# Kernel optimization log

Hardware: AMD Instinct MI355X
Metric: run time of the kernel (lower is better)

Reference implementation:

```python
import jax, jax.numpy as jnp
import numpy as np

STATE_DIM = 512
N_AGENTS = 16
N_ACTIONS = 32
EMBED = 512          # mixing_embed_dim
Q_IN = STATE_DIM + N_AGENTS * N_ACTIONS  # 1024 (coma_critic arch)
ROWS = 32768         # bs * ts = 64 * 512


def _linear_params(key, d_in, d_out):
    kw, kb = jax.random.split(key)
    bound = 1.0 / np.sqrt(d_in)
    W = jax.random.uniform(kw, (d_in, d_out), minval=-bound, maxval=bound, dtype=jnp.float32)
    b = jax.random.uniform(kb, (d_out,), minval=-bound, maxval=bound, dtype=jnp.float32)
    return W, b


def setup_inputs() -> dict:
    key = jax.random.key(0)
    ks = jax.random.split(key, 8)
    states = jax.random.normal(ks[0], (ROWS, STATE_DIM), dtype=jnp.float32)
    actions = jax.random.uniform(ks[1], (ROWS, N_AGENTS * N_ACTIONS), dtype=jnp.float32)
    Qw1, Qb1 = _linear_params(ks[2], Q_IN, EMBED)
    Qw2, Qb2 = _linear_params(ks[3], EMBED, EMBED)
    Qw3, Qb3 = _linear_params(ks[4], EMBED, 1)
    Vw1, Vb1 = _linear_params(ks[5], STATE_DIM, EMBED)
    Vw2, Vb2 = _linear_params(ks[6], EMBED, EMBED)
    Vw3, Vb3 = _linear_params(ks[7], EMBED, 1)
    return {
        "states": states, "actions": actions,
        "Qw1": Qw1, "Qb1": Qb1, "Qw2": Qw2, "Qb2": Qb2, "Qw3": Qw3, "Qb3": Qb3,
        "Vw1": Vw1, "Vb1": Vb1, "Vw2": Vw2, "Vb2": Vb2, "Vw3": Vw3, "Vb3": Vb3,
    }


def _mlp3(x, W1, b1, W2, b2, W3, b3):
    h = jax.nn.relu(x @ W1 + b1)
    h = jax.nn.relu(h @ W2 + b2)
    return h @ W3 + b3


def reference(states, actions,
              Qw1, Qb1, Qw2, Qb2, Qw3, Qb3,
              Vw1, Vb1, Vw2, Vb2, Vw3, Vb3):
    # coma_critic arch: inputs = cat([states, joint-action one-hots], dim=1)
    inputs = jnp.concatenate([states, actions], axis=1)  # [bs*ts, Q_IN]
    q_outputs = _mlp3(inputs, Qw1, Qb1, Qw2, Qb2, Qw3, Qb3)  # [bs*ts, 1]
    v_outputs = _mlp3(states, Vw1, Vb1, Vw2, Vb2, Vw3, Vb3)  # [bs*ts, 1]
    return q_outputs, v_outputs
```

## Files before the change

### kernel.cpp

```cpp
#include <hip/hip_runtime.h>


#define ROWS 32768
#define EMBED 512

using frag_ab = __attribute__((ext_vector_type(8))) short;
using f32x4   = __attribute__((ext_vector_type(4))) float;

__device__ __forceinline__ unsigned short f2bf(float f) {
    unsigned int u = __builtin_bit_cast(unsigned int, f);
    return (unsigned short)((u + 0x7fffu + ((u >> 16) & 1u)) >> 16);
}

__device__ __forceinline__ unsigned pk2(float lo, float hi) {
    return __builtin_amdgcn_perm(__builtin_bit_cast(unsigned, hi),
                                 __builtin_bit_cast(unsigned, lo), 0x07060302u);
}

__device__ __forceinline__ void async_copy16(const void* g, void* l) {
    __builtin_amdgcn_global_load_lds(
        (const __attribute__((address_space(1))) unsigned int*)g,
        (__attribute__((address_space(3))) unsigned int*)l, 16, 0, 0);
}

__global__ void init_out(float* __restrict__ out,
                         const float* __restrict__ qb3,
                         const float* __restrict__ vb3) {
    int i = blockIdx.x * 256 + threadIdx.x;
    out[i] = (i < ROWS) ? qb3[0] : vb3[0];
}

__global__ void prep_w(const float* __restrict__ Qw1, const float* __restrict__ Qw2,
                       const float* __restrict__ Vw1, const float* __restrict__ Vw2,
                       unsigned short* __restrict__ Qw1t, unsigned short* __restrict__ Qw2t,
                       unsigned short* __restrict__ Vw1t, unsigned short* __restrict__ Vw2t) {
    int t = blockIdx.x * 256 + threadIdx.x;
    if (t < 512 * 1024) {
        int n = t >> 10, k = t & 1023;
        Qw1t[t] = f2bf(Qw1[(size_t)k * 512 + n]);
    } else {
        t -= 512 * 1024;
        int seg = t >> 18;
        int r = t & 0x3ffff;
        int n = r >> 9, k = r & 511;
        const float* W = (seg == 0) ? Qw2 : (seg == 1) ? Vw1 : Vw2;
        unsigned short* O = (seg == 0) ? Qw2t : (seg == 1) ? Vw1t : Vw2t;
        O[r] = f2bf(W[(size_t)k * 512 + n]);
    }
}

__global__ __launch_bounds__(256)
void layer1(const float* __restrict__ states, const float* __restrict__ actions,
            const unsigned short* __restrict__ Qw1t,
            const unsigned short* __restrict__ Vw1t,
            const float* __restrict__ Qb1, const float* __restrict__ Vb1,
            unsigned short* __restrict__ h1Q, unsigned short* __restrict__ h1V) {
    __shared__ __align__(16) unsigned short As[128 * 40];
    __shared__ __align__(16) unsigned short Bs[128 * 32];

    const int tid = threadIdx.x, wave = tid >> 6, lane = tid & 63;
    const bool isV = blockIdx.x >= 4;
    const int bn = (blockIdx.x & 3) * 128;
    const int bm = blockIdx.y * 128;
    const int K   = isV ? 512 : 1024;
    const int ldb = isV ? 512 : 1024;
    const unsigned short* Wt = isV ? Vw1t : Qw1t;
    const float* bias = isV ? Vb1 : Qb1;
    unsigned short* H = isV ? h1V : h1Q;

    const int wm = (wave & 1) * 64, wn = (wave >> 1) * 64;
    const int lrow = lane & 15, quad = lane >> 4;
    f32x4 acc[4][4] = {};

    const int lin  = wave * 1024 + lane * 16;
    const int rowS = lin >> 6, colS = (lin & 63) >> 1;
    const unsigned short* gB0 = Wt + (size_t)(bn + rowS)      * ldb + colS;
    const unsigned short* gB1 = Wt + (size_t)(bn + rowS + 64) * ldb + colS;
    unsigned short* ldsB0 = Bs + wave * 512;
    unsigned short* ldsB1 = Bs + 2048 + wave * 512;

    const int arow = tid >> 1, ahalf = tid & 1;
    const size_t rowOff = (size_t)(bm + arow) * 512 + ahalf * 16;
    unsigned short* wp = As + arow * 40 + ahalf * 16;

    float4 f0, f1, f2, f3;
    { const float4* g = (const float4*)(states + rowOff);
      f0 = g[0]; f1 = g[1]; f2 = g[2]; f3 = g[3]; }

    for (int k0 = 0; k0 < K; k0 += 32) {
        async_copy16(gB0, ldsB0);
        async_copy16(gB1, ldsB1);
        gB0 += 32; gB1 += 32;
        uint4 w0 = make_uint4(pk2(f0.x, f0.y), pk2(f0.z, f0.w),
                              pk2(f1.x, f1.y), pk2(f1.z, f1.w));
        uint4 w1 = make_uint4(pk2(f2.x, f2.y), pk2(f2.z, f2.w),
                              pk2(f3.x, f3.y), pk2(f3.z, f3.w));
        *(uint4*)wp       = w0;
        *(uint4*)(wp + 8) = w1;
        __syncthreads();

        const int kn = k0 + 32;
        if (kn < K) {
            const float* Ab = (kn < 512) ? states : actions;
            const float4* g = (const float4*)(Ab + rowOff + (kn & 511));
            f0 = g[0]; f1 = g[1]; f2 = g[2]; f3 = g[3];
        }

        frag_ab af[4], bfr[4];
#pragma unroll
        for (int i = 0; i < 4; i++)
            af[i] = *(const frag_ab*)&As[(wm + i * 16 + lrow) * 40 + quad * 8];
#pragma unroll
        for (int j = 0; j < 4; j++)
            bfr[j] = *(const frag_ab*)&Bs[(wn + j * 16 + lrow) * 32 + quad * 8];
#pragma unroll
        for (int i = 0; i < 4; i++)
#pragma unroll
            for (int j = 0; j < 4; j++)
                acc[i][j] = __builtin_amdgcn_mfma_f32_16x16x32_bf16(
                    af[i], bfr[j], acc[i][j], 0, 0, 0);
        __syncthreads();
    }

#pragma unroll
    for (int j = 0; j < 4; j++) {
        const int col = bn + wn + j * 16 + lrow;
        const float bc = bias[col];
#pragma unroll
        for (int i = 0; i < 4; i++) {
            const int row0 = bm + wm + i * 16 + quad * 4;
#pragma unroll
            for (int r = 0; r < 4; r++) {
                float v = acc[i][j][r] + bc;
                v = v > 0.0f ? v : 0.0f;
                H[(size_t)(row0 + r) * EMBED + col] = f2bf(v);
            }
        }
    }
}

__global__ __launch_bounds__(256)
void layer2(const unsigned short* __restrict__ h1Q,
            const unsigned short* __restrict__ h1V,
            const unsigned short* __restrict__ Qw2t,
            const unsigned short* __restrict__ Vw2t,
            const float* __restrict__ Qb2, const float* __restrict__ Vb2,
            const float* __restrict__ Qw3, const float* __restrict__ Vw3,
            float* __restrict__ out) {
    __shared__ __align__(16) unsigned short As[128 * 32];
    __shared__ __align__(16) unsigned short Bs[128 * 32];

    const int tid = threadIdx.x, wave = tid >> 6, lane = tid & 63;
    const bool isV = blockIdx.x >= 4;
    const int bn = (blockIdx.x & 3) * 128;
    const int bm = blockIdx.y * 128;
    const unsigned short* A  = isV ? h1V : h1Q;
    const unsigned short* Wt = isV ? Vw2t : Qw2t;
    const float* bias = isV ? Vb2 : Qb2;
    const float* w3   = isV ? Vw3 : Qw3;
    float* op = out + (isV ? ROWS : 0);

    const int wm = (wave & 1) * 64, wn = (wave >> 1) * 64;
    const int lrow = lane & 15, quad = lane >> 4;
    f32x4 acc[4][4] = {};

    const int lin  = wave * 1024 + lane * 16;
    const int rowS = lin >> 6, colS = (lin & 63) >> 1;
    const unsigned short* gA0 = A  + (size_t)(bm + rowS)      * 512 + colS;
    const unsigned short* gA1 = A  + (size_t)(bm + rowS + 64) * 512 + colS;
    const unsigned short* gB0 = Wt + (size_t)(bn + rowS)      * 512 + colS;
    const unsigned short* gB1 = Wt + (size_t)(bn + rowS + 64) * 512 + colS;
    unsigned short* ldsA0 = As + wave * 512;
    unsigned short* ldsA1 = As + 2048 + wave * 512;
    unsigned short* ldsB0 = Bs + wave * 512;
    unsigned short* ldsB1 = Bs + 2048 + wave * 512;

    for (int k0 = 0; k0 < 512; k0 += 32) {
        async_copy16(gA0, ldsA0);
        async_copy16(gA1, ldsA1);
        async_copy16(gB0, ldsB0);
        async_copy16(gB1, ldsB1);
        gA0 += 32; gA1 += 32; gB0 += 32; gB1 += 32;
        __syncthreads();

        frag_ab af[4], bfr[4];
#pragma unroll
        for (int i = 0; i < 4; i++)
            af[i] = *(const frag_ab*)&As[(wm + i * 16 + lrow) * 32 + quad * 8];
#pragma unroll
        for (int j = 0; j < 4; j++)
            bfr[j] = *(const frag_ab*)&Bs[(wn + j * 16 + lrow) * 32 + quad * 8];
#pragma unroll
        for (int i = 0; i < 4; i++)
#pragma unroll
            for (int j = 0; j < 4; j++)
                acc[i][j] = __builtin_amdgcn_mfma_f32_16x16x32_bf16(
                    af[i], bfr[j], acc[i][j], 0, 0, 0);
        __syncthreads();
    }

    float bc[4], wc[4];
#pragma unroll
    for (int j = 0; j < 4; j++) {
        const int col = bn + wn + j * 16 + lrow;
        bc[j] = bias[col];
        wc[j] = w3[col];
    }
#pragma unroll
    for (int i = 0; i < 4; i++) {
#pragma unroll
        for (int r = 0; r < 4; r++) {
            float s = 0.0f;
#pragma unroll
            for (int j = 0; j < 4; j++) {
                float v = acc[i][j][r] + bc[j];
                v = v > 0.0f ? v : 0.0f;
                s += v * wc[j];
            }
#pragma unroll
            for (int m = 1; m < 16; m <<= 1) s += __shfl_xor(s, m, 64);
            if (lrow == 0)
                atomicAdd(&op[bm + wm + i * 16 + quad * 4 + r], s);
        }
    }
}

extern "C" void kernel_launch(void* const* d_in, const int* in_sizes, int n_in,
                              void* d_out, int out_size, void* d_ws, size_t ws_size,
                              hipStream_t stream) {
    const float* states  = (const float*)d_in[0];
    const float* actions = (const float*)d_in[1];
    const float* Qw1 = (const float*)d_in[2];
    const float* Qb1 = (const float*)d_in[3];
    const float* Qw2 = (const float*)d_in[4];
    const float* Qb2 = (const float*)d_in[5];
    const float* Qw3 = (const float*)d_in[6];
    const float* Qb3 = (const float*)d_in[7];
    const float* Vw1 = (const float*)d_in[8];
    const float* Vb1 = (const float*)d_in[9];
    const float* Vw2 = (const float*)d_in[10];
    const float* Vb2 = (const float*)d_in[11];
    const float* Vw3 = (const float*)d_in[12];
    const float* Vb3 = (const float*)d_in[13];
    float* out = (float*)d_out;

    char* ws = (char*)d_ws;
    unsigned short* h1Q  = (unsigned short*)ws;
    unsigned short* h1V  = (unsigned short*)(ws + 33554432);
    unsigned short* Qw1t = (unsigned short*)(ws + 67108864);
    unsigned short* Qw2t = Qw1t + 512 * 1024;
    unsigned short* Vw1t = Qw2t + 512 * 512;
    unsigned short* Vw2t = Vw1t + 512 * 512;

    init_out<<<dim3(256), dim3(256), 0, stream>>>(out, Qb3, Vb3);
    prep_w<<<dim3(5120), dim3(256), 0, stream>>>(Qw1, Qw2, Vw1, Vw2,
                                                 Qw1t, Qw2t, Vw1t, Vw2t);

    dim3 grid(8, ROWS / 128);
    layer1<<<grid, 256, 0, stream>>>(states, actions, Qw1t, Vw1t,
                                     Qb1, Vb1, h1Q, h1V);
    layer2<<<grid, 256, 0, stream>>>(h1Q, h1V, Qw2t, Vw2t,
                                     Qb2, Vb2, Qw3, Vw3, out);
}
```

Measured before the change: 352.0 us.

## Pre-convert activations to bf16 buffer and async-load A tiles in layer1

```diff
diff --git a/kernel.cpp b/kernel.cpp
--- a/kernel.cpp
+++ b/kernel.cpp
@@ -12,9 +12,8 @@
     return (unsigned short)((u + 0x7fffu + ((u >> 16) & 1u)) >> 16);
 }
 
-__device__ __forceinline__ unsigned pk2(float lo, float hi) {
-    return __builtin_amdgcn_perm(__builtin_bit_cast(unsigned, hi),
-                                 __builtin_bit_cast(unsigned, lo), 0x07060302u);
+__device__ __forceinline__ unsigned pk2rne(float lo, float hi) {
+    return (unsigned)f2bf(lo) | ((unsigned)f2bf(hi) << 16);
 }
 
 __device__ __forceinline__ void async_copy16(const void* g, void* l) {
@@ -23,47 +22,69 @@
         (__attribute__((address_space(3))) unsigned int*)l, 16, 0, 0);
 }
 
-__global__ void init_out(float* __restrict__ out,
-                         const float* __restrict__ qb3,
-                         const float* __restrict__ vb3) {
-    int i = blockIdx.x * 256 + threadIdx.x;
-    out[i] = (i < ROWS) ? qb3[0] : vb3[0];
-}
-
-__global__ void prep_w(const float* __restrict__ Qw1, const float* __restrict__ Qw2,
-                       const float* __restrict__ Vw1, const float* __restrict__ Vw2,
-                       unsigned short* __restrict__ Qw1t, unsigned short* __restrict__ Qw2t,
-                       unsigned short* __restrict__ Vw1t, unsigned short* __restrict__ Vw2t) {
-    int t = blockIdx.x * 256 + threadIdx.x;
-    if (t < 512 * 1024) {
-        int n = t >> 10, k = t & 1023;
-        Qw1t[t] = f2bf(Qw1[(size_t)k * 512 + n]);
+__global__ __launch_bounds__(256)
+void prep(const float* __restrict__ states, const float* __restrict__ actions,
+          const float* __restrict__ Qw1, const float* __restrict__ Qw2,
+          const float* __restrict__ Vw1, const float* __restrict__ Vw2,
+          const float* __restrict__ qb3, const float* __restrict__ vb3,
+          unsigned short* __restrict__ X,
+          unsigned short* __restrict__ Qw1t, unsigned short* __restrict__ Qw2t,
+          unsigned short* __restrict__ Vw1t, unsigned short* __restrict__ Vw2t,
+          float* __restrict__ out) {
+    const int b = blockIdx.x, tid = threadIdx.x;
+    if (b < 4096) {
+        int c = b * 256 + tid;
+        int m = c >> 5, col = (c & 31) * 32;
+        const float* src = (col < 512) ? states + (size_t)m * 512 + col
+                                       : actions + (size_t)m * 512 + (col - 512);
+        float4 f[8];
+#pragma unroll
+        for (int i = 0; i < 8; i++) f[i] = ((const float4*)src)[i];
+        uint4* dst = (uint4*)(X + (size_t)m * 1024 + col);
+#pragma unroll
+        for (int i = 0; i < 4; i++)
+            dst[i] = make_uint4(pk2rne(f[2*i].x,   f[2*i].y),
+                                pk2rne(f[2*i].z,   f[2*i].w),
+                                pk2rne(f[2*i+1].x, f[2*i+1].y),
+                                pk2rne(f[2*i+1].z, f[2*i+1].w));
+    } else if (b < 4736) {
+        int g = (b - 4096) * 256 + tid;
+        const float* W; unsigned short* O; int n, k0, ldo;
+        if (g < 65536) {
+            int o = g * 8; n = o >> 10; k0 = o & 1023; W = Qw1; O = Qw1t; ldo = 1024;
+        } else {
+            g -= 65536;
+            int seg = g >> 15, r = g & 32767, o = r * 8;
+            n = o >> 9; k0 = o & 511; ldo = 512;
+            W = (seg == 0) ? Qw2 : (seg == 1) ? Vw1 : Vw2;
+            O = (seg == 0) ? Qw2t : (seg == 1) ? Vw1t : Vw2t;
+        }
+        float v[8];
+#pragma unroll
+        for (int j = 0; j < 8; j++) v[j] = W[(size_t)(k0 + j) * 512 + n];
+        *(uint4*)(O + (size_t)n * ldo + k0) =
+            make_uint4(pk2rne(v[0], v[1]), pk2rne(v[2], v[3]),
+                       pk2rne(v[4], v[5]), pk2rne(v[6], v[7]));
     } else {
-        t -= 512 * 1024;
-        int seg = t >> 18;
-        int r = t & 0x3ffff;
-        int n = r >> 9, k = r & 511;
-        const float* W = (seg == 0) ? Qw2 : (seg == 1) ? Vw1 : Vw2;
-        unsigned short* O = (seg == 0) ? Qw2t : (seg == 1) ? Vw1t : Vw2t;
-        O[r] = f2bf(W[(size_t)k * 512 + n]);
+        int i = (b - 4736) * 256 + tid;
+        out[i] = (i < ROWS) ? qb3[0] : vb3[0];
     }
 }
 
 __global__ __launch_bounds__(256)
-void layer1(const float* __restrict__ states, const float* __restrict__ actions,
+void layer1(const unsigned short* __restrict__ X,
             const unsigned short* __restrict__ Qw1t,
             const unsigned short* __restrict__ Vw1t,
             const float* __restrict__ Qb1, const float* __restrict__ Vb1,
             unsigned short* __restrict__ h1Q, unsigned short* __restrict__ h1V) {
-    __shared__ __align__(16) unsigned short As[128 * 40];
+    __shared__ __align__(16) unsigned short As[128 * 32];
     __shared__ __align__(16) unsigned short Bs[128 * 32];
 
     const int tid = threadIdx.x, wave = tid >> 6, lane = tid & 63;
     const bool isV = blockIdx.x >= 4;
     const int bn = (blockIdx.x & 3) * 128;
     const int bm = blockIdx.y * 128;
-    const int K   = isV ? 512 : 1024;
-    const int ldb = isV ? 512 : 1024;
+    const int K = isV ? 512 : 1024;
     const unsigned short* Wt = isV ? Vw1t : Qw1t;
     const float* bias = isV ? Vb1 : Qb1;
     unsigned short* H = isV ? h1V : h1Q;
@@ -74,42 +95,27 @@
 
     const int lin  = wave * 1024 + lane * 16;
     const int rowS = lin >> 6, colS = (lin & 63) >> 1;
-    const unsigned short* gB0 = Wt + (size_t)(bn + rowS)      * ldb + colS;
-    const unsigned short* gB1 = Wt + (size_t)(bn + rowS + 64) * ldb + colS;
+    const unsigned short* gA0 = X  + (size_t)(bm + rowS)      * 1024 + colS;
+    const unsigned short* gA1 = X  + (size_t)(bm + rowS + 64) * 1024 + colS;
+    const unsigned short* gB0 = Wt + (size_t)(bn + rowS)      * K + colS;
+    const unsigned short* gB1 = Wt + (size_t)(bn + rowS + 64) * K + colS;
+    unsigned short* ldsA0 = As + wave * 512;
+    unsigned short* ldsA1 = As + 2048 + wave * 512;
     unsigned short* ldsB0 = Bs + wave * 512;
     unsigned short* ldsB1 = Bs + 2048 + wave * 512;
 
-    const int arow = tid >> 1, ahalf = tid & 1;
-    const size_t rowOff = (size_t)(bm + arow) * 512 + ahalf * 16;
-    unsigned short* wp = As + arow * 40 + ahalf * 16;
-
-    float4 f0, f1, f2, f3;
-    { const float4* g = (const float4*)(states + rowOff);
-      f0 = g[0]; f1 = g[1]; f2 = g[2]; f3 = g[3]; }
-
     for (int k0 = 0; k0 < K; k0 += 32) {
+        async_copy16(gA0, ldsA0);
+        async_copy16(gA1, ldsA1);
         async_copy16(gB0, ldsB0);
         async_copy16(gB1, ldsB1);
-        gB0 += 32; gB1 += 32;
-        uint4 w0 = make_uint4(pk2(f0.x, f0.y), pk2(f0.z, f0.w),
-                              pk2(f1.x, f1.y), pk2(f1.z, f1.w));
-        uint4 w1 = make_uint4(pk2(f2.x, f2.y), pk2(f2.z, f2.w),
-                              pk2(f3.x, f3.y), pk2(f3.z, f3.w));
-        *(uint4*)wp       = w0;
-        *(uint4*)(wp + 8) = w1;
-        __syncthreads();
-
-        const int kn = k0 + 32;
-        if (kn < K) {
-            const float* Ab = (kn < 512) ? states : actions;
-            const float4* g = (const float4*)(Ab + rowOff + (kn & 511));
-            f0 = g[0]; f1 = g[1]; f2 = g[2]; f3 = g[3];
-        }
+        gA0 += 32; gA1 += 32; gB0 += 32; gB1 += 32;
+        __syncthreads();
 
         frag_ab af[4], bfr[4];
 #pragma unroll
         for (int i = 0; i < 4; i++)
-            af[i] = *(const frag_ab*)&As[(wm + i * 16 + lrow) * 40 + quad * 8];
+            af[i] = *(const frag_ab*)&As[(wm + i * 16 + lrow) * 32 + quad * 8];
 #pragma unroll
         for (int j = 0; j < 4; j++)
             bfr[j] = *(const frag_ab*)&Bs[(wn + j * 16 + lrow) * 32 + quad * 8];
@@ -245,20 +251,18 @@
     float* out = (float*)d_out;
 
     char* ws = (char*)d_ws;
-    unsigned short* h1Q  = (unsigned short*)ws;
-    unsigned short* h1V  = (unsigned short*)(ws + 33554432);
-    unsigned short* Qw1t = (unsigned short*)(ws + 67108864);
+    unsigned short* X    = (unsigned short*)ws;
+    unsigned short* h1Q  = (unsigned short*)(ws + 67108864);
+    unsigned short* h1V  = (unsigned short*)(ws + 100663296);
+    unsigned short* Qw1t = (unsigned short*)(ws + 134217728);
     unsigned short* Qw2t = Qw1t + 512 * 1024;
     unsigned short* Vw1t = Qw2t + 512 * 512;
     unsigned short* Vw2t = Vw1t + 512 * 512;
 
-    init_out<<<dim3(256), dim3(256), 0, stream>>>(out, Qb3, Vb3);
-    prep_w<<<dim3(5120), dim3(256), 0, stream>>>(Qw1, Qw2, Vw1, Vw2,
-                                                 Qw1t, Qw2t, Vw1t, Vw2t);
+    prep<<<dim3(4992), dim3(256), 0, stream>>>(states, actions, Qw1, Qw2, Vw1, Vw2,
+                                               Qb3, Vb3, X, Qw1t, Qw2t, Vw1t, Vw2t, out);
 
     dim3 grid(8, ROWS / 128);
-    layer1<<<grid, 256, 0, stream>>>(states, actions, Qw1t, Vw1t,
-                                     Qb1, Vb1, h1Q, h1V);
-    layer2<<<grid, 256, 0, stream>>>(h1Q, h1V, Qw2t, Vw2t,
-                                     Qb2, Vb2, Qw3, Vw3, out);
-}
+    layer1<<<grid, 256, 0, stream>>>(X, Qw1t, Vw1t, Qb1, Vb1, h1Q, h1V);
+    layer2<<<grid, 256, 0, stream>>>(h1Q, h1V, Qw2t, Vw2t, Qb2, Vb2, Qw3, Vw3, out);
+}
```

Result: faster. 337.8 us (-4.0%).
